# Optimization experiments

Measured on AMD Instinct MI355X. Metric: run time of the kernel, lower is better.

Reference implementation:

```python
import jax, jax.numpy as jnp
import numpy as np

N, E, F, H, C = 50000, 800000, 128, 256, 40
BN_EPS = 1e-5


def setup_inputs() -> dict:
    key = jax.random.key(0)
    ks = jax.random.split(key, 8)
    s = 0.05
    return {
        'x': jax.random.normal(ks[0], (N, F), jnp.float32),
        'edge_index': jax.random.randint(ks[1], (2, E), 0, N),
        'eps1': jnp.zeros((), jnp.float32),
        'W1': jax.random.normal(ks[2], (F, H), jnp.float32) * s,
        'b1': jnp.zeros((H,), jnp.float32),
        'g1': jnp.ones((H,), jnp.float32),
        'be1': jnp.zeros((H,), jnp.float32),
        'W2': jax.random.normal(ks[3], (H, H), jnp.float32) * s,
        'b2': jnp.zeros((H,), jnp.float32),
        'eps2': jnp.zeros((), jnp.float32),
        'W3': jax.random.normal(ks[4], (H, H), jnp.float32) * s,
        'b3': jnp.zeros((H,), jnp.float32),
        'g2': jnp.ones((H,), jnp.float32),
        'be2': jnp.zeros((H,), jnp.float32),
        'W4': jax.random.normal(ks[5], (H, H), jnp.float32) * s,
        'b4': jnp.zeros((H,), jnp.float32),
        'g3': jnp.ones((H,), jnp.float32),
        'be3': jnp.zeros((H,), jnp.float32),
        'Wf': jax.random.normal(ks[6], (H, C), jnp.float32) * s,
        'bf': jnp.zeros((C,), jnp.float32),
    }


def _bn(h, g, b):
    # BatchNorm1d forward with batch statistics (training-mode math, biased var)
    m = jnp.mean(h, axis=0)
    v = jnp.var(h, axis=0)
    return (h - m) * jax.lax.rsqrt(v + BN_EPS) * g + b


def _gin_conv(x, edge_index, eps, Wa, ba, g, be, Wb, bb):
    # GINConv: out = mlp((1+eps)*x + sum_{(src->dst)} x[src])
    src, dst = edge_index[0], edge_index[1]
    agg = jax.ops.segment_sum(x[src], dst, num_segments=x.shape[0])  # [N, d]
    h = (1.0 + eps) * x + agg
    h = jnp.maximum(_bn(h @ Wa + ba, g, be), 0.0)  # Linear-BN-ReLU
    return h @ Wb + bb                              # Linear


def reference(x, edge_index, eps1, W1, b1, g1, be1, W2, b2,
              eps2, W3, b3, g2, be2, W4, b4, g3, be3, Wf, bf):
    h = _gin_conv(x, edge_index, eps1, W1, b1, g1, be1, W2, b2)
    h = jnp.maximum(h, 0.0)  # F.relu (dropout p=0)
    h = _gin_conv(h, edge_index, eps2, W3, b3, g2, be2, W4, b4)
    h = jnp.maximum(_bn(h, g3, be3), 0.0)  # bn2 + relu
    return h @ Wf + bf  # fc -> [N, C]
```

## Files before the change

### kernel.cpp

```cpp
#include <hip/hip_runtime.h>
#include <hip/hip_bf16.h>


#define NN 50000
#define EE 800000
#define FDIM 128
#define HDIM 256
#define CDIM 40
#define BN_EPS 1e-5f
#define CSTRIDE 136

typedef unsigned short u16;
typedef unsigned int u32;
typedef __attribute__((ext_vector_type(8))) short short8;
typedef __attribute__((ext_vector_type(4))) float f32x4;

__device__ __forceinline__ float bflo(u32 u) { return __uint_as_float(u << 16); }
__device__ __forceinline__ float bfhi(u32 u) { return __uint_as_float(u & 0xFFFF0000u); }
__device__ __forceinline__ u16 f2bf(float f) {
  __hip_bfloat16 h = __float2bfloat16(f);
  return *(u16*)&h;
}
__device__ __forceinline__ u32 pack2(float a, float b) {
  return (u32)f2bf(a) | ((u32)f2bf(b) << 16);
}

__global__ void k_hist(const int* __restrict__ ei, int* __restrict__ deg) {
  int e = blockIdx.x * 256 + threadIdx.x;
  if (e < EE) atomicAdd(&deg[ei[EE + e]], 1);
}

__global__ void k_scan_blocks(const int* __restrict__ in, int* __restrict__ partial,
                              int* __restrict__ bsums, int n) {
  __shared__ int s[256];
  int i = blockIdx.x * 256 + threadIdx.x;
  s[threadIdx.x] = (i < n) ? in[i] : 0;
  __syncthreads();
  for (int d = 1; d < 256; d <<= 1) {
    int t = (threadIdx.x >= d) ? s[threadIdx.x - d] : 0;
    __syncthreads();
    s[threadIdx.x] += t;
    __syncthreads();
  }
  if (i < n) partial[i] = s[threadIdx.x];
  if (threadIdx.x == 255) bsums[blockIdx.x] = s[255];
}

__global__ void k_scan_sums(int* __restrict__ bs, int nb) {
  __shared__ int s[256];
  s[threadIdx.x] = (threadIdx.x < nb) ? bs[threadIdx.x] : 0;
  __syncthreads();
  for (int d = 1; d < 256; d <<= 1) {
    int t = (threadIdx.x >= d) ? s[threadIdx.x - d] : 0;
    __syncthreads();
    s[threadIdx.x] += t;
    __syncthreads();
  }
  int ex = (threadIdx.x == 0) ? 0 : s[threadIdx.x - 1];
  if (threadIdx.x < nb) bs[threadIdx.x] = ex;
}

__global__ void k_scan_add(const int* __restrict__ partial, const int* __restrict__ bs,
                           int* __restrict__ rowstart, int n) {
  int i = blockIdx.x * 256 + threadIdx.x;
  if (i < n) rowstart[i + 1] = partial[i] + bs[blockIdx.x];
  if (i == 0) rowstart[0] = 0;
}

__global__ void k_copy_i32(const int* __restrict__ a, int* __restrict__ b, int n) {
  int i = blockIdx.x * 256 + threadIdx.x;
  if (i < n) b[i] = a[i];
}

__global__ void k_scatter(const int* __restrict__ ei, int* __restrict__ cursor,
                          int* __restrict__ sorted_src) {
  int e = blockIdx.x * 256 + threadIdx.x;
  if (e < EE) {
    int dst = ei[EE + e];
    int p = atomicAdd(&cursor[dst], 1);
    sorted_src[p] = ei[e];
  }
}

__global__ void k_cvt_x(const float* __restrict__ x, u16* __restrict__ xb) {
  int i = blockIdx.x * 256 + threadIdx.x;
  size_t base = (size_t)i * 4;
  if (base < (size_t)NN * FDIM) {
    float4 v = *(const float4*)&x[base];
    u32 lo = pack2(v.x, v.y), hi = pack2(v.z, v.w);
    *(uint2*)&xb[base] = make_uint2(lo, hi);
  }
}

__global__ void k_cvt_wt(const float* __restrict__ W, u16* __restrict__ Wt, int K) {
  int i = blockIdx.x * 256 + threadIdx.x;
  int k = i >> 8, n = i & 255;
  if (k < K) Wt[(size_t)n * K + k] = f2bf(W[i]);
}

template <int FEAT>
__global__ __launch_bounds__(256)
void k_agg(const u16* __restrict__ x, const int* __restrict__ rowstart,
           const int* __restrict__ sorted_src, const float* __restrict__ epsp,
           u16* __restrict__ out) {
  int node = blockIdx.x * 4 + (threadIdx.x >> 6);
  if (node >= NN) return;
  int lane = threadIdx.x & 63;
  float e1 = 1.0f + epsp[0];
  int s = rowstart[node], t = rowstart[node + 1];
  if constexpr (FEAT == 128) {
    const u32* xp = (const u32*)x;
    u32 u = xp[(size_t)node * 64 + lane];
    float a0 = bflo(u) * e1, a1 = bfhi(u) * e1;
    int p = s;
    for (; p + 7 < t; p += 8) {
      u32 uu[8];
#pragma unroll
      for (int i = 0; i < 8; ++i) uu[i] = xp[(size_t)sorted_src[p + i] * 64 + lane];
#pragma unroll
      for (int i = 0; i < 8; ++i) { a0 += bflo(uu[i]); a1 += bfhi(uu[i]); }
    }
    for (; p + 1 < t; p += 2) {
      u32 u0 = xp[(size_t)sorted_src[p] * 64 + lane];
      u32 u1 = xp[(size_t)sorted_src[p + 1] * 64 + lane];
      a0 += bflo(u0) + bflo(u1);
      a1 += bfhi(u0) + bfhi(u1);
    }
    if (p < t) {
      u32 u0 = xp[(size_t)sorted_src[p] * 64 + lane];
      a0 += bflo(u0); a1 += bfhi(u0);
    }
    ((u32*)out)[(size_t)node * 64 + lane] = pack2(a0, a1);
  } else {
    const uint2* xp = (const uint2*)x;
    uint2 u = xp[(size_t)node * 64 + lane];
    float a0 = bflo(u.x) * e1, a1 = bfhi(u.x) * e1;
    float a2 = bflo(u.y) * e1, a3 = bfhi(u.y) * e1;
    int p = s;
    for (; p + 7 < t; p += 8) {
      uint2 uu[8];
#pragma unroll
      for (int i = 0; i < 8; ++i) uu[i] = xp[(size_t)sorted_src[p + i] * 64 + lane];
#pragma unroll
      for (int i = 0; i < 8; ++i) {
        a0 += bflo(uu[i].x); a1 += bfhi(uu[i].x);
        a2 += bflo(uu[i].y); a3 += bfhi(uu[i].y);
      }
    }
    for (; p + 1 < t; p += 2) {
      uint2 u0 = xp[(size_t)sorted_src[p] * 64 + lane];
      uint2 u1 = xp[(size_t)sorted_src[p + 1] * 64 + lane];
      a0 += bflo(u0.x) + bflo(u1.x);
      a1 += bfhi(u0.x) + bfhi(u1.x);
      a2 += bflo(u0.y) + bflo(u1.y);
      a3 += bfhi(u0.y) + bfhi(u1.y);
    }
    if (p < t) {
      uint2 u0 = xp[(size_t)sorted_src[p] * 64 + lane];
      a0 += bflo(u0.x); a1 += bfhi(u0.x);
      a2 += bflo(u0.y); a3 += bfhi(u0.y);
    }
    ((uint2*)out)[(size_t)node * 64 + lane] = make_uint2(pack2(a0, a1), pack2(a2, a3));
  }
}

template <int K, bool TRANSFORM, bool RELU_OUT, bool COLSUMS>
__global__ __launch_bounds__(256)
void k_gemm(const u16* __restrict__ A, const u16* __restrict__ Bt,
            const float* __restrict__ bias, const float* __restrict__ ta,
            const float* __restrict__ tc, u16* __restrict__ C,
            float* __restrict__ csum, float* __restrict__ csq) {
  constexpr int NCH = K / 8;
  constexpr int NKS = K / 32;
  constexpr int NTILE = (NN + 31) / 32;
  __shared__ u16 Bs[128 * K];
  __shared__ u16 Cs[32 * CSTRIDE];
  __shared__ float2 Tb[K];

  const int tid = threadIdx.x;
  const int lane = tid & 63;
  const int w = tid >> 6;
  const int wm = w >> 1, wn = w & 1;
  const int lr = lane & 15, lq = lane >> 4;
  const int half = blockIdx.x & 1;
  const u16* Bth = Bt + (size_t)half * 128 * K;

  for (int i = tid; i < 128 * NCH; i += 256) {
    int row = i / NCH, c = i % NCH;
    short8 v = *(const short8*)&Bth[(size_t)row * K + c * 8];
    ((short8*)Bs)[row * NCH + (c ^ (row & 7))] = v;
  }
  if constexpr (TRANSFORM) {
    for (int k = tid; k < K; k += 256) Tb[k] = make_float2(ta[k], tc[k]);
  }

  float bv[4];
#pragma unroll
  for (int ni = 0; ni < 4; ++ni) bv[ni] = bias[half * 128 + wn * 64 + ni * 16 + lr];
  float colS[4] = {}, colQ[4] = {};

  __syncthreads();

  short8 bufA[NKS], bufB[NKS];

  auto LOADA = [&](short8* dst, int rt) {
    int row = rt * 32 + wm * 16 + lr;
    int rowc = row < NN ? row : NN - 1;
    const u16* Ap = &A[(size_t)rowc * K];
#pragma unroll
    for (int ks = 0; ks < NKS; ++ks)
      dst[ks] = *(const short8*)&Ap[ks * 32 + lq * 8];
  };

  auto BODY = [&](short8* cur, short8* nxt, int rt) {
    if constexpr (TRANSFORM) {
#pragma unroll
      for (int ks = 0; ks < NKS; ++ks) {
        short8 v = cur[ks];
#pragma unroll
        for (int j = 0; j < 8; ++j) {
          float2 tb = Tb[ks * 32 + lq * 8 + j];
          float f = __uint_as_float(((u32)(u16)v[j]) << 16);
          v[j] = (short)f2bf(fmaxf(fmaf(f, tb.x, tb.y), 0.f));
        }
        cur[ks] = v;
      }
    }
    if (rt + 256 < NTILE) LOADA(nxt, rt + 256);

    f32x4 acc[4];
#pragma unroll
    for (int ni = 0; ni < 4; ++ni) acc[ni] = (f32x4){0.f, 0.f, 0.f, 0.f};
    __builtin_amdgcn_s_setprio(1);
#pragma unroll
    for (int ks = 0; ks < NKS; ++ks) {
#pragma unroll
      for (int ni = 0; ni < 4; ++ni) {
        int col = wn * 64 + ni * 16 + lr;
        int c = (ks * 4 + lq) ^ (col & 7);
        short8 bfr = ((const short8*)Bs)[col * NCH + c];
        acc[ni] = __builtin_amdgcn_mfma_f32_16x16x32_bf16(cur[ks], bfr, acc[ni], 0, 0, 0);
      }
    }
    __builtin_amdgcn_s_setprio(0);

#pragma unroll
    for (int ni = 0; ni < 4; ++ni) {
      int col = wn * 64 + ni * 16 + lr;
#pragma unroll
      for (int j = 0; j < 4; ++j) {
        int r = wm * 16 + lq * 4 + j;
        float v = acc[ni][j] + bv[ni];
        if constexpr (RELU_OUT) v = fmaxf(v, 0.f);
        if constexpr (COLSUMS) {
          if (rt * 32 + r < NN) { colS[ni] += v; colQ[ni] += v * v; }
        }
        Cs[r * CSTRIDE + col] = f2bf(v);
      }
    }
    __syncthreads();
    {
      int r = tid >> 3;
      int gr = rt * 32 + r;
      if (gr < NN) {
        const uint4* src = (const uint4*)&Cs[r * CSTRIDE + (tid & 7) * 16];
        uint4 v0 = src[0], v1 = src[1];
        uint4* dst = (uint4*)&C[(size_t)gr * HDIM + half * 128 + (tid & 7) * 16];
        dst[0] = v0; dst[1] = v1;
      }
    }
    __syncthreads();
  };

  LOADA(bufA, blockIdx.x >> 1);
  for (int rt = blockIdx.x >> 1; rt < NTILE; rt += 512) {
    BODY(bufA, bufB, rt);
    if (rt + 256 < NTILE) BODY(bufB, bufA, rt + 256);
  }

  if constexpr (COLSUMS) {
#pragma unroll
    for (int ni = 0; ni < 4; ++ni) {
      float s = colS[ni], q = colQ[ni];
      s += __shfl_xor(s, 16); s += __shfl_xor(s, 32);
      q += __shfl_xor(q, 16); q += __shfl_xor(q, 32);
      if (lq == 0) {
        int col = half * 128 + wn * 64 + ni * 16 + lr;
        atomicAdd(&csum[col], s);
        atomicAdd(&csq[col], q);
      }
    }
  }
}

__global__ void k_bn_fin(const float* __restrict__ sum, const float* __restrict__ sq,
                         const float* __restrict__ g, const float* __restrict__ be,
                         float* __restrict__ a, float* __restrict__ c) {
  int t = threadIdx.x;
  float m = sum[t] * (1.0f / NN);
  float var = sq[t] * (1.0f / NN) - m * m;
  float s = g[t] * rsqrtf(var + BN_EPS);
  a[t] = s;
  c[t] = be[t] - m * s;
}

__global__ __launch_bounds__(256)
void k_gemm_final(const u16* __restrict__ A, const float* __restrict__ B,
                  const float* __restrict__ bias, const float* __restrict__ ta,
                  const float* __restrict__ tc, float* __restrict__ C) {
  __shared__ float As[64][65];
  __shared__ float Bs[64][CDIM];
  int tid = threadIdx.x;
  int r = tid & 63, q = tid >> 6;
  int r0 = blockIdx.x * 64;
  float acc[10] = {};
  for (int k0 = 0; k0 < HDIM; k0 += 64) {
#pragma unroll
    for (int i = 0; i < 4; ++i) {
      int idx = tid + i * 256;
      int row = idx >> 4;
      int c4 = (idx & 15) * 4;
      int gr = r0 + row;
      float v0 = 0.f, v1 = 0.f, v2 = 0.f, v3 = 0.f;
      if (gr < NN) {
        uint2 u = *(const uint2*)&A[(size_t)gr * HDIM + k0 + c4];
        v0 = fmaxf(fmaf(bflo(u.x), ta[k0 + c4 + 0], tc[k0 + c4 + 0]), 0.f);
        v1 = fmaxf(fmaf(bfhi(u.x), ta[k0 + c4 + 1], tc[k0 + c4 + 1]), 0.f);
        v2 = fmaxf(fmaf(bflo(u.y), ta[k0 + c4 + 2], tc[k0 + c4 + 2]), 0.f);
        v3 = fmaxf(fmaf(bfhi(u.y), ta[k0 + c4 + 3], tc[k0 + c4 + 3]), 0.f);
      }
      As[c4 + 0][row] = v0;
      As[c4 + 1][row] = v1;
      As[c4 + 2][row] = v2;
      As[c4 + 3][row] = v3;
    }
#pragma unroll
    for (int i = 0; i < 10; ++i) {
      int idx = tid + i * 256;
      int row = idx / CDIM;
      int col = idx % CDIM;
      Bs[row][col] = B[(size_t)(k0 + row) * CDIM + col];
    }
    __syncthreads();
#pragma unroll
    for (int k = 0; k < 64; ++k) {
      float a = As[k][r];
#pragma unroll
      for (int j = 0; j < 10; ++j) acc[j] = fmaf(a, Bs[k][q * 10 + j], acc[j]);
    }
    __syncthreads();
  }
  int gr = r0 + r;
  if (gr < NN) {
#pragma unroll
    for (int j = 0; j < 10; ++j) C[(size_t)gr * CDIM + q * 10 + j] = acc[j] + bias[q * 10 + j];
  }
}

extern "C" void kernel_launch(void* const* d_in, const int* in_sizes, int n_in,
                              void* d_out, int out_size, void* d_ws, size_t ws_size,
                              hipStream_t stream) {
  const float* x   = (const float*)d_in[0];
  const int*   ei  = (const int*)d_in[1];
  const float* eps1= (const float*)d_in[2];
  const float* W1  = (const float*)d_in[3];
  const float* b1  = (const float*)d_in[4];
  const float* g1  = (const float*)d_in[5];
  const float* be1 = (const float*)d_in[6];
  const float* W2  = (const float*)d_in[7];
  const float* b2  = (const float*)d_in[8];
  const float* eps2= (const float*)d_in[9];
  const float* W3  = (const float*)d_in[10];
  const float* b3  = (const float*)d_in[11];
  const float* g2  = (const float*)d_in[12];
  const float* be2 = (const float*)d_in[13];
  const float* W4  = (const float*)d_in[14];
  const float* b4  = (const float*)d_in[15];
  const float* g3  = (const float*)d_in[16];
  const float* be3 = (const float*)d_in[17];
  const float* Wf  = (const float*)d_in[18];
  const float* bf  = (const float*)d_in[19];
  float* out = (float*)d_out;

  char* p = (char*)d_ws;
  auto alloc = [&](size_t bytes) -> char* {
    char* r = p;
    p += (bytes + 255) & ~(size_t)255;
    return r;
  };
  float* stats   = (float*)alloc(12 * 256 * sizeof(float));
  int* deg       = (int*)alloc(NN * sizeof(int));
  int* rowstart  = (int*)alloc((NN + 16) * sizeof(int));
  int* cursor    = (int*)alloc(NN * sizeof(int));
  int* sorted    = (int*)alloc(EE * sizeof(int));
  int* partial   = (int*)alloc(NN * sizeof(int));
  int* bsums     = (int*)alloc(1024 * sizeof(int));
  u16* W1t       = (u16*)alloc(256 * 128 * sizeof(u16));
  u16* W2t       = (u16*)alloc(256 * 256 * sizeof(u16));
  u16* W3t       = (u16*)alloc(256 * 256 * sizeof(u16));
  u16* W4t       = (u16*)alloc(256 * 256 * sizeof(u16));
  u16* xb        = (u16*)alloc((size_t)NN * 128 * sizeof(u16));
  u16* A1        = (u16*)alloc((size_t)NN * 128 * sizeof(u16));
  u16* z1        = (u16*)alloc((size_t)NN * 256 * sizeof(u16));
  u16* h1        = (u16*)alloc((size_t)NN * 256 * sizeof(u16));
  u16* A2        = (u16*)alloc((size_t)NN * 256 * sizeof(u16));
  (void)alloc(64 * 1024);
  u16* z2 = z1;
  u16* z3 = h1;

  hipMemsetAsync(deg, 0, NN * sizeof(int), stream);
  hipMemsetAsync(stats, 0, 12 * 256 * sizeof(float), stream);

  const int nbE = (EE + 255) / 256;
  const int nbN = (NN + 255) / 256;

  k_hist<<<nbE, 256, 0, stream>>>(ei, deg);
  k_scan_blocks<<<nbN, 256, 0, stream>>>(deg, partial, bsums, NN);
  k_scan_sums<<<1, 256, 0, stream>>>(bsums, nbN);
  k_scan_add<<<nbN, 256, 0, stream>>>(partial, bsums, rowstart, NN);
  k_copy_i32<<<nbN, 256, 0, stream>>>(rowstart, cursor, NN);
  k_scatter<<<nbE, 256, 0, stream>>>(ei, cursor, sorted);

  k_cvt_x<<<(NN * FDIM / 4 + 255) / 256, 256, 0, stream>>>(x, xb);
  k_cvt_wt<<<128, 256, 0, stream>>>(W1, W1t, 128);
  k_cvt_wt<<<256, 256, 0, stream>>>(W2, W2t, 256);
  k_cvt_wt<<<256, 256, 0, stream>>>(W3, W3t, 256);
  k_cvt_wt<<<256, 256, 0, stream>>>(W4, W4t, 256);

  k_agg<128><<<(NN + 3) / 4, 256, 0, stream>>>(xb, rowstart, sorted, eps1, A1);
  k_gemm<128, false, false, true><<<512, 256, 0, stream>>>(
      A1, W1t, b1, nullptr, nullptr, z1, stats + 0, stats + 256);
  k_bn_fin<<<1, 256, 0, stream>>>(stats + 0, stats + 256, g1, be1,
                                  stats + 2 * 256, stats + 3 * 256);
  k_gemm<256, true, true, false><<<512, 256, 0, stream>>>(
      z1, W2t, b2, stats + 2 * 256, stats + 3 * 256, h1, nullptr, nullptr);

  k_agg<256><<<(NN + 3) / 4, 256, 0, stream>>>(h1, rowstart, sorted, eps2, A2);
  k_gemm<256, false, false, true><<<512, 256, 0, stream>>>(
      A2, W3t, b3, nullptr, nullptr, z2, stats + 4 * 256, stats + 5 * 256);
  k_bn_fin<<<1, 256, 0, stream>>>(stats + 4 * 256, stats + 5 * 256, g2, be2,
                                  stats + 6 * 256, stats + 7 * 256);
  k_gemm<256, true, false, true><<<512, 256, 0, stream>>>(
      z2, W4t, b4, stats + 6 * 256, stats + 7 * 256, z3, stats + 8 * 256, stats + 9 * 256);
  k_bn_fin<<<1, 256, 0, stream>>>(stats + 8 * 256, stats + 9 * 256, g3, be3,
                                  stats + 10 * 256, stats + 11 * 256);

  k_gemm_final<<<(NN + 63) / 64, 256, 0, stream>>>(
      z3, Wf, bf, stats + 10 * 256, stats + 11 * 256, out);
}
```

Measured before the change: 391.4 us.

## Fuse neighbor aggregation into GEMM, fold BN finalize, use MFMA for final layer

The edge aggregation now runs inside a new 1024-thread GEMM kernel that gathers 32 rows into shared memory and multiplies them there, which removes the A1/A2 intermediate round trips through global memory. The BN finalize kernels are folded into the consuming GEMMs, the weight conversions are merged into a single launch, and the final fp32 FMA GEMM is replaced by a bf16 MFMA kernel using a padded transposed Wf. The cost is a 1024-thread block holding the full B matrix in LDS, which lowers occupancy and ties the gather latency to each tile's MFMA schedule. The final layer also gains an extra bf16 rounding.

Measured after the change: 378.3 us. 1.03x faster.

```diff
diff --git a/kernel.cpp b/kernel.cpp
--- a/kernel.cpp
+++ b/kernel.cpp
@@ -87,89 +87,234 @@
   size_t base = (size_t)i * 4;
   if (base < (size_t)NN * FDIM) {
     float4 v = *(const float4*)&x[base];
-    u32 lo = pack2(v.x, v.y), hi = pack2(v.z, v.w);
-    *(uint2*)&xb[base] = make_uint2(lo, hi);
-  }
-}
-
-__global__ void k_cvt_wt(const float* __restrict__ W, u16* __restrict__ Wt, int K) {
-  int i = blockIdx.x * 256 + threadIdx.x;
-  int k = i >> 8, n = i & 255;
-  if (k < K) Wt[(size_t)n * K + k] = f2bf(W[i]);
-}
-
-template <int FEAT>
-__global__ __launch_bounds__(256)
-void k_agg(const u16* __restrict__ x, const int* __restrict__ rowstart,
-           const int* __restrict__ sorted_src, const float* __restrict__ epsp,
-           u16* __restrict__ out) {
-  int node = blockIdx.x * 4 + (threadIdx.x >> 6);
-  if (node >= NN) return;
-  int lane = threadIdx.x & 63;
-  float e1 = 1.0f + epsp[0];
-  int s = rowstart[node], t = rowstart[node + 1];
-  if constexpr (FEAT == 128) {
-    const u32* xp = (const u32*)x;
-    u32 u = xp[(size_t)node * 64 + lane];
-    float a0 = bflo(u) * e1, a1 = bfhi(u) * e1;
-    int p = s;
-    for (; p + 7 < t; p += 8) {
-      u32 uu[8];
-#pragma unroll
-      for (int i = 0; i < 8; ++i) uu[i] = xp[(size_t)sorted_src[p + i] * 64 + lane];
-#pragma unroll
-      for (int i = 0; i < 8; ++i) { a0 += bflo(uu[i]); a1 += bfhi(uu[i]); }
-    }
-    for (; p + 1 < t; p += 2) {
-      u32 u0 = xp[(size_t)sorted_src[p] * 64 + lane];
-      u32 u1 = xp[(size_t)sorted_src[p + 1] * 64 + lane];
-      a0 += bflo(u0) + bflo(u1);
-      a1 += bfhi(u0) + bfhi(u1);
-    }
-    if (p < t) {
-      u32 u0 = xp[(size_t)sorted_src[p] * 64 + lane];
-      a0 += bflo(u0); a1 += bfhi(u0);
-    }
-    ((u32*)out)[(size_t)node * 64 + lane] = pack2(a0, a1);
+    *(uint2*)&xb[base] = make_uint2(pack2(v.x, v.y), pack2(v.z, v.w));
+  }
+}
+
+__global__ void k_cvt_w(const float* __restrict__ W1, const float* __restrict__ W2,
+                        const float* __restrict__ W3, const float* __restrict__ W4,
+                        const float* __restrict__ Wf,
+                        u16* __restrict__ W1t, u16* __restrict__ W2t,
+                        u16* __restrict__ W3t, u16* __restrict__ W4t,
+                        u16* __restrict__ Wft) {
+  int b = blockIdx.x, t = threadIdx.x;
+  if (b < 128) {
+    int i = b * 256 + t; int k = i >> 8, n = i & 255;
+    W1t[(size_t)n * 128 + k] = f2bf(W1[i]);
+  } else if (b < 384) {
+    int i = (b - 128) * 256 + t; int k = i >> 8, n = i & 255;
+    W2t[(size_t)n * 256 + k] = f2bf(W2[i]);
+  } else if (b < 640) {
+    int i = (b - 384) * 256 + t; int k = i >> 8, n = i & 255;
+    W3t[(size_t)n * 256 + k] = f2bf(W3[i]);
+  } else if (b < 896) {
+    int i = (b - 640) * 256 + t; int k = i >> 8, n = i & 255;
+    W4t[(size_t)n * 256 + k] = f2bf(W4[i]);
   } else {
-    const uint2* xp = (const uint2*)x;
-    uint2 u = xp[(size_t)node * 64 + lane];
-    float a0 = bflo(u.x) * e1, a1 = bfhi(u.x) * e1;
-    float a2 = bflo(u.y) * e1, a3 = bfhi(u.y) * e1;
-    int p = s;
-    for (; p + 7 < t; p += 8) {
-      uint2 uu[8];
-#pragma unroll
-      for (int i = 0; i < 8; ++i) uu[i] = xp[(size_t)sorted_src[p + i] * 64 + lane];
-#pragma unroll
-      for (int i = 0; i < 8; ++i) {
-        a0 += bflo(uu[i].x); a1 += bfhi(uu[i].x);
-        a2 += bflo(uu[i].y); a3 += bfhi(uu[i].y);
-      }
-    }
-    for (; p + 1 < t; p += 2) {
-      uint2 u0 = xp[(size_t)sorted_src[p] * 64 + lane];
-      uint2 u1 = xp[(size_t)sorted_src[p + 1] * 64 + lane];
-      a0 += bflo(u0.x) + bflo(u1.x);
-      a1 += bfhi(u0.x) + bfhi(u1.x);
-      a2 += bflo(u0.y) + bflo(u1.y);
-      a3 += bfhi(u0.y) + bfhi(u1.y);
-    }
-    if (p < t) {
-      uint2 u0 = xp[(size_t)sorted_src[p] * 64 + lane];
-      a0 += bflo(u0.x); a1 += bfhi(u0.x);
-      a2 += bflo(u0.y); a3 += bfhi(u0.y);
-    }
-    ((uint2*)out)[(size_t)node * 64 + lane] = make_uint2(pack2(a0, a1), pack2(a2, a3));
-  }
-}
-
-template <int K, bool TRANSFORM, bool RELU_OUT, bool COLSUMS>
+    int i = (b - 896) * 256 + t;
+    int c = i >> 8, k = i & 255;
+    Wft[(size_t)c * 256 + k] = (c < CDIM) ? f2bf(Wf[(size_t)k * CDIM + c]) : (u16)0;
+  }
+}
+
+template <int K>
+__global__ __launch_bounds__(1024)
+void k_fused(const u16* __restrict__ X, const int* __restrict__ rowstart,
+             const int* __restrict__ sorted_src, const float* __restrict__ epsp,
+             const u16* __restrict__ Bt, const float* __restrict__ bias,
+             u16* __restrict__ C, float* __restrict__ csum, float* __restrict__ csq) {
+  constexpr int NCH = K / 8;
+  constexpr bool DB = (K == 128);
+  constexpr int NTILE = (NN + 31) / 32;
+  __shared__ u16 Bs[256 * K];
+  __shared__ u16 As[DB ? 2 : 1][32 * K];
+  __shared__ u16 Cs[DB ? 32 * 272 : 8];
+
+  const int tid = threadIdx.x;
+  const int lane = tid & 63;
+  const int w = tid >> 6;
+  const int rg = w >> 3, cg = w & 7;
+  const int lr = lane & 15, lq = lane >> 4;
+
+  for (int i = tid; i < 256 * NCH; i += 1024) {
+    int row = i / NCH, c = i % NCH;
+    ((short8*)Bs)[row * NCH + (c ^ (row & 7))] = ((const short8*)Bt)[i];
+  }
+  const float e1 = 1.0f + epsp[0];
+  float bv[2];
+#pragma unroll
+  for (int ni = 0; ni < 2; ++ni) bv[ni] = bias[cg * 32 + ni * 16 + lr];
+  float colS[2] = {}, colQ[2] = {};
+
+  auto GATHER = [&](int grow, float* a) {
+    a[0] = a[1] = 0.f;
+    if constexpr (!DB) { a[2] = a[3] = 0.f; }
+    if (grow >= NN) return;
+    int s = rowstart[grow], t = rowstart[grow + 1];
+    if constexpr (!DB) {
+      const uint2* xp = (const uint2*)X;
+      uint2 u = xp[(size_t)grow * 64 + lane];
+      a[0] = bflo(u.x) * e1; a[1] = bfhi(u.x) * e1;
+      a[2] = bflo(u.y) * e1; a[3] = bfhi(u.y) * e1;
+      int p = s;
+      for (; p + 7 < t; p += 8) {
+        uint2 uu[8];
+#pragma unroll
+        for (int i = 0; i < 8; ++i) uu[i] = xp[(size_t)sorted_src[p + i] * 64 + lane];
+#pragma unroll
+        for (int i = 0; i < 8; ++i) {
+          a[0] += bflo(uu[i].x); a[1] += bfhi(uu[i].x);
+          a[2] += bflo(uu[i].y); a[3] += bfhi(uu[i].y);
+        }
+      }
+      for (; p < t; ++p) {
+        uint2 u0 = xp[(size_t)sorted_src[p] * 64 + lane];
+        a[0] += bflo(u0.x); a[1] += bfhi(u0.x);
+        a[2] += bflo(u0.y); a[3] += bfhi(u0.y);
+      }
+    } else {
+      const u32* xp = (const u32*)X;
+      u32 u = xp[(size_t)grow * 64 + lane];
+      a[0] = bflo(u) * e1; a[1] = bfhi(u) * e1;
+      int p = s;
+      for (; p + 7 < t; p += 8) {
+        u32 uu[8];
+#pragma unroll
+        for (int i = 0; i < 8; ++i) uu[i] = xp[(size_t)sorted_src[p + i] * 64 + lane];
+#pragma unroll
+        for (int i = 0; i < 8; ++i) { a[0] += bflo(uu[i]); a[1] += bfhi(uu[i]); }
+      }
+      for (; p < t; ++p) {
+        u32 u0 = xp[(size_t)sorted_src[p] * 64 + lane];
+        a[0] += bflo(u0); a[1] += bfhi(u0);
+      }
+    }
+  };
+
+  auto GWRITE = [&](u16* Abuf, int lw, const float* a) {
+    if constexpr (!DB) {
+      int idx = lw * 256 + (((lane >> 1) ^ (lw & 7)) << 3) + (lane & 1) * 4;
+      *(uint2*)&Abuf[idx] = make_uint2(pack2(a[0], a[1]), pack2(a[2], a[3]));
+    } else {
+      int idx = lw * 128 + (((lane >> 2) ^ (lw & 7)) << 3) + (lane & 3) * 2;
+      *(u32*)&Abuf[idx] = pack2(a[0], a[1]);
+    }
+  };
+
+  const int arow = rg * 16 + lr;
+  auto MFMA_TILE = [&](const u16* Abuf, f32x4* acc) {
+    acc[0] = (f32x4){0.f, 0.f, 0.f, 0.f};
+    acc[1] = (f32x4){0.f, 0.f, 0.f, 0.f};
+    __builtin_amdgcn_s_setprio(1);
+#pragma unroll
+    for (int ks = 0; ks < K / 32; ++ks) {
+      short8 af = *(const short8*)&Abuf[arow * K + (((ks * 4 + lq) ^ (arow & 7)) << 3)];
+#pragma unroll
+      for (int ni = 0; ni < 2; ++ni) {
+        int col = cg * 32 + ni * 16 + lr;
+        short8 bfr = ((const short8*)Bs)[col * NCH + ((ks * 4 + lq) ^ (col & 7))];
+        acc[ni] = __builtin_amdgcn_mfma_f32_16x16x32_bf16(af, bfr, acc[ni], 0, 0, 0);
+      }
+    }
+    __builtin_amdgcn_s_setprio(0);
+  };
+
+  const int rt0 = blockIdx.x;
+  float ga0[4], ga1[4];
+  GATHER(rt0 * 32 + w * 2 + 0, ga0);
+  GATHER(rt0 * 32 + w * 2 + 1, ga1);
+  GWRITE(As[0], w * 2 + 0, ga0);
+  GWRITE(As[0], w * 2 + 1, ga1);
+  __syncthreads();
+
+  int cur = 0;
+  for (int rt = rt0; rt < NTILE; rt += 256) {
+    f32x4 acc[2];
+    MFMA_TILE(As[cur], acc);
+    bool hn = (rt + 256) < NTILE;
+    if (hn) {
+      GATHER((rt + 256) * 32 + w * 2 + 0, ga0);
+      GATHER((rt + 256) * 32 + w * 2 + 1, ga1);
+    }
+    if constexpr (DB) {
+#pragma unroll
+      for (int ni = 0; ni < 2; ++ni) {
+        int col = cg * 32 + ni * 16 + lr;
+#pragma unroll
+        for (int j = 0; j < 4; ++j) {
+          int r = rg * 16 + lq * 4 + j;
+          float v = acc[ni][j] + bv[ni];
+          if (rt * 32 + r < NN) { colS[ni] += v; colQ[ni] += v * v; }
+          Cs[r * 272 + col] = f2bf(v);
+        }
+      }
+      if (hn) {
+        GWRITE(As[cur ^ 1], w * 2 + 0, ga0);
+        GWRITE(As[cur ^ 1], w * 2 + 1, ga1);
+      }
+      __syncthreads();
+      {
+        int r = tid >> 5, ch = tid & 31;
+        int gr = rt * 32 + r;
+        if (gr < NN) {
+          uint4 v = *(const uint4*)&Cs[r * 272 + ch * 8];
+          *(uint4*)&C[(size_t)gr * 256 + ch * 8] = v;
+        }
+      }
+      __syncthreads();
+      cur ^= 1;
+    } else {
+      __syncthreads();
+#pragma unroll
+      for (int ni = 0; ni < 2; ++ni) {
+        int col = cg * 32 + ni * 16 + lr;
+#pragma unroll
+        for (int j = 0; j < 4; ++j) {
+          int r = rg * 16 + lq * 4 + j;
+          float v = acc[ni][j] + bv[ni];
+          if (rt * 32 + r < NN) { colS[ni] += v; colQ[ni] += v * v; }
+          As[0][r * 256 + (((col >> 3) ^ (r & 7)) << 3) + (col & 7)] = f2bf(v);
+        }
+      }
+      __syncthreads();
+      {
+        int r = tid >> 5, ch = tid & 31;
+        int gr = rt * 32 + r;
+        if (gr < NN) {
+          uint4 v = *(const uint4*)&As[0][r * 256 + ((ch ^ (r & 7)) << 3)];
+          *(uint4*)&C[(size_t)gr * 256 + ch * 8] = v;
+        }
+      }
+      __syncthreads();
+      if (hn) {
+        GWRITE(As[0], w * 2 + 0, ga0);
+        GWRITE(As[0], w * 2 + 1, ga1);
+      }
+      __syncthreads();
+    }
+  }
+
+#pragma unroll
+  for (int ni = 0; ni < 2; ++ni) {
+    float s = colS[ni], q = colQ[ni];
+    s += __shfl_xor(s, 16); s += __shfl_xor(s, 32);
+    q += __shfl_xor(q, 16); q += __shfl_xor(q, 32);
+    if (lq == 0) {
+      int col = cg * 32 + ni * 16 + lr;
+      atomicAdd(&csum[col], s);
+      atomicAdd(&csq[col], q);
+    }
+  }
+}
+
+template <bool RELU_OUT, bool COLSUMS>
 __global__ __launch_bounds__(256)
 void k_gemm(const u16* __restrict__ A, const u16* __restrict__ Bt,
-            const float* __restrict__ bias, const float* __restrict__ ta,
-            const float* __restrict__ tc, u16* __restrict__ C,
-            float* __restrict__ csum, float* __restrict__ csq) {
+            const float* __restrict__ bias,
+            const float* __restrict__ icsum, const float* __restrict__ icsq,
+            const float* __restrict__ g, const float* __restrict__ be,
+            u16* __restrict__ C, float* __restrict__ ocsum, float* __restrict__ ocsq) {
+  constexpr int K = 256;
   constexpr int NCH = K / 8;
   constexpr int NKS = K / 32;
   constexpr int NTILE = (NN + 31) / 32;
@@ -190,8 +335,11 @@
     short8 v = *(const short8*)&Bth[(size_t)row * K + c * 8];
     ((short8*)Bs)[row * NCH + (c ^ (row & 7))] = v;
   }
-  if constexpr (TRANSFORM) {
-    for (int k = tid; k < K; k += 256) Tb[k] = make_float2(ta[k], tc[k]);
+  if (tid < 256) {
+    float m = icsum[tid] * (1.0f / NN);
+    float var = icsq[tid] * (1.0f / NN) - m * m;
+    float s = g[tid] * rsqrtf(var + BN_EPS);
+    Tb[tid] = make_float2(s, be[tid] - m * s);
   }
 
   float bv[4];
@@ -213,18 +361,16 @@
   };
 
   auto BODY = [&](short8* cur, short8* nxt, int rt) {
-    if constexpr (TRANSFORM) {
-#pragma unroll
-      for (int ks = 0; ks < NKS; ++ks) {
-        short8 v = cur[ks];
-#pragma unroll
-        for (int j = 0; j < 8; ++j) {
-          float2 tb = Tb[ks * 32 + lq * 8 + j];
-          float f = __uint_as_float(((u32)(u16)v[j]) << 16);
-          v[j] = (short)f2bf(fmaxf(fmaf(f, tb.x, tb.y), 0.f));
-        }
-        cur[ks] = v;
-      }
+#pragma unroll
+    for (int ks = 0; ks < NKS; ++ks) {
+      short8 v = cur[ks];
+#pragma unroll
+      for (int j = 0; j < 8; ++j) {
+        float2 tb = Tb[ks * 32 + lq * 8 + j];
+        float f = __uint_as_float(((u32)(u16)v[j]) << 16);
+        v[j] = (short)f2bf(fmaxf(fmaf(f, tb.x, tb.y), 0.f));
+      }
+      cur[ks] = v;
     }
     if (rt + 256 < NTILE) LOADA(nxt, rt + 256);
 
@@ -286,74 +432,78 @@
       q += __shfl_xor(q, 16); q += __shfl_xor(q, 32);
       if (lq == 0) {
         int col = half * 128 + wn * 64 + ni * 16 + lr;
-        atomicAdd(&csum[col], s);
-        atomicAdd(&csq[col], q);
-      }
-    }
-  }
-}
-
-__global__ void k_bn_fin(const float* __restrict__ sum, const float* __restrict__ sq,
-                         const float* __restrict__ g, const float* __restrict__ be,
-                         float* __restrict__ a, float* __restrict__ c) {
-  int t = threadIdx.x;
-  float m = sum[t] * (1.0f / NN);
-  float var = sq[t] * (1.0f / NN) - m * m;
-  float s = g[t] * rsqrtf(var + BN_EPS);
-  a[t] = s;
-  c[t] = be[t] - m * s;
+        atomicAdd(&ocsum[col], s);
+        atomicAdd(&ocsq[col], q);
+      }
+    }
+  }
 }
 
 __global__ __launch_bounds__(256)
-void k_gemm_final(const u16* __restrict__ A, const float* __restrict__ B,
-                  const float* __restrict__ bias, const float* __restrict__ ta,
-                  const float* __restrict__ tc, float* __restrict__ C) {
-  __shared__ float As[64][65];
-  __shared__ float Bs[64][CDIM];
-  int tid = threadIdx.x;
-  int r = tid & 63, q = tid >> 6;
-  int r0 = blockIdx.x * 64;
-  float acc[10] = {};
-  for (int k0 = 0; k0 < HDIM; k0 += 64) {
-#pragma unroll
-    for (int i = 0; i < 4; ++i) {
-      int idx = tid + i * 256;
-      int row = idx >> 4;
-      int c4 = (idx & 15) * 4;
-      int gr = r0 + row;
-      float v0 = 0.f, v1 = 0.f, v2 = 0.f, v3 = 0.f;
-      if (gr < NN) {
-        uint2 u = *(const uint2*)&A[(size_t)gr * HDIM + k0 + c4];
-        v0 = fmaxf(fmaf(bflo(u.x), ta[k0 + c4 + 0], tc[k0 + c4 + 0]), 0.f);
-        v1 = fmaxf(fmaf(bfhi(u.x), ta[k0 + c4 + 1], tc[k0 + c4 + 1]), 0.f);
-        v2 = fmaxf(fmaf(bflo(u.y), ta[k0 + c4 + 2], tc[k0 + c4 + 2]), 0.f);
-        v3 = fmaxf(fmaf(bfhi(u.y), ta[k0 + c4 + 3], tc[k0 + c4 + 3]), 0.f);
-      }
-      As[c4 + 0][row] = v0;
-      As[c4 + 1][row] = v1;
-      As[c4 + 2][row] = v2;
-      As[c4 + 3][row] = v3;
-    }
-#pragma unroll
-    for (int i = 0; i < 10; ++i) {
-      int idx = tid + i * 256;
-      int row = idx / CDIM;
-      int col = idx % CDIM;
-      Bs[row][col] = B[(size_t)(k0 + row) * CDIM + col];
-    }
-    __syncthreads();
-#pragma unroll
-    for (int k = 0; k < 64; ++k) {
-      float a = As[k][r];
-#pragma unroll
-      for (int j = 0; j < 10; ++j) acc[j] = fmaf(a, Bs[k][q * 10 + j], acc[j]);
-    }
-    __syncthreads();
-  }
-  int gr = r0 + r;
-  if (gr < NN) {
-#pragma unroll
-    for (int j = 0; j < 10; ++j) C[(size_t)gr * CDIM + q * 10 + j] = acc[j] + bias[q * 10 + j];
+void k_final(const u16* __restrict__ z3, const u16* __restrict__ Wft,
+             const float* __restrict__ bf,
+             const float* __restrict__ icsum, const float* __restrict__ icsq,
+             const float* __restrict__ g, const float* __restrict__ be,
+             float* __restrict__ out) {
+  __shared__ u16 Bs[48 * 256];
+  __shared__ float2 Tb[256];
+  const int tid = threadIdx.x;
+  const int lane = tid & 63;
+  const int w = tid >> 6;
+  const int lr = lane & 15, lq = lane >> 4;
+
+  for (int i = tid; i < 48 * 32; i += 256) {
+    int row = i >> 5, c = i & 31;
+    ((short8*)Bs)[row * 32 + (c ^ (row & 7))] = ((const short8*)Wft)[i];
+  }
+  if (tid < 256) {
+    float m = icsum[tid] * (1.0f / NN);
+    float var = icsq[tid] * (1.0f / NN) - m * m;
+    float s = g[tid] * rsqrtf(var + BN_EPS);
+    Tb[tid] = make_float2(s, be[tid] - m * s);
+  }
+  __syncthreads();
+
+  int row = blockIdx.x * 64 + w * 16 + lr;
+  int rowc = row < NN ? row : NN - 1;
+  const u16* Ap = &z3[(size_t)rowc * 256];
+  short8 a[8];
+#pragma unroll
+  for (int ks = 0; ks < 8; ++ks) {
+    short8 v = *(const short8*)&Ap[ks * 32 + lq * 8];
+#pragma unroll
+    for (int j = 0; j < 8; ++j) {
+      float2 tb = Tb[ks * 32 + lq * 8 + j];
+      float f = __uint_as_float(((u32)(u16)v[j]) << 16);
+      v[j] = (short)f2bf(fmaxf(fmaf(f, tb.x, tb.y), 0.f));
+    }
+    a[ks] = v;
+  }
+
+  f32x4 acc[3];
+#pragma unroll
+  for (int ni = 0; ni < 3; ++ni) acc[ni] = (f32x4){0.f, 0.f, 0.f, 0.f};
+#pragma unroll
+  for (int ks = 0; ks < 8; ++ks) {
+#pragma unroll
+    for (int ni = 0; ni < 3; ++ni) {
+      int col = ni * 16 + lr;
+      short8 bfr = ((const short8*)Bs)[col * 32 + ((ks * 4 + lq) ^ (col & 7))];
+      acc[ni] = __builtin_amdgcn_mfma_f32_16x16x32_bf16(a[ks], bfr, acc[ni], 0, 0, 0);
+    }
+  }
+
+#pragma unroll
+  for (int ni = 0; ni < 3; ++ni) {
+    int col = ni * 16 + lr;
+    if (col < CDIM) {
+      float bfv = bf[col];
+#pragma unroll
+      for (int j = 0; j < 4; ++j) {
+        int gr = blockIdx.x * 64 + w * 16 + lq * 4 + j;
+        if (gr < NN) out[(size_t)gr * CDIM + col] = acc[ni][j] + bfv;
+      }
+    }
   }
 }
 
@@ -388,7 +538,7 @@
     p += (bytes + 255) & ~(size_t)255;
     return r;
   };
-  float* stats   = (float*)alloc(12 * 256 * sizeof(float));
+  float* stats   = (float*)alloc(6 * 256 * sizeof(float));
   int* deg       = (int*)alloc(NN * sizeof(int));
   int* rowstart  = (int*)alloc((NN + 16) * sizeof(int));
   int* cursor    = (int*)alloc(NN * sizeof(int));
@@ -399,17 +549,20 @@
   u16* W2t       = (u16*)alloc(256 * 256 * sizeof(u16));
   u16* W3t       = (u16*)alloc(256 * 256 * sizeof(u16));
   u16* W4t       = (u16*)alloc(256 * 256 * sizeof(u16));
+  u16* Wft       = (u16*)alloc(48 * 256 * sizeof(u16));
   u16* xb        = (u16*)alloc((size_t)NN * 128 * sizeof(u16));
-  u16* A1        = (u16*)alloc((size_t)NN * 128 * sizeof(u16));
   u16* z1        = (u16*)alloc((size_t)NN * 256 * sizeof(u16));
   u16* h1        = (u16*)alloc((size_t)NN * 256 * sizeof(u16));
-  u16* A2        = (u16*)alloc((size_t)NN * 256 * sizeof(u16));
   (void)alloc(64 * 1024);
   u16* z2 = z1;
   u16* z3 = h1;
 
+  float* s1 = stats + 0,    *q1 = stats + 256;
+  float* s2 = stats + 512,  *q2 = stats + 768;
+  float* s3 = stats + 1024, *q3 = stats + 1280;
+
   hipMemsetAsync(deg, 0, NN * sizeof(int), stream);
-  hipMemsetAsync(stats, 0, 12 * 256 * sizeof(float), stream);
+  hipMemsetAsync(stats, 0, 6 * 256 * sizeof(float), stream);
 
   const int nbE = (EE + 255) / 256;
   const int nbN = (NN + 255) / 256;
@@ -422,29 +575,11 @@
   k_scatter<<<nbE, 256, 0, stream>>>(ei, cursor, sorted);
 
   k_cvt_x<<<(NN * FDIM / 4 + 255) / 256, 256, 0, stream>>>(x, xb);
-  k_cvt_wt<<<128, 256, 0, stream>>>(W1, W1t, 128);
-  k_cvt_wt<<<256, 256, 0, stream>>>(W2, W2t, 256);
-  k_cvt_wt<<<256, 256, 0, stream>>>(W3, W3t, 256);
-  k_cvt_wt<<<256, 256, 0, stream>>>(W4, W4t, 256);
-
-  k_agg<128><<<(NN + 3) / 4, 256, 0, stream>>>(xb, rowstart, sorted, eps1, A1);
-  k_gemm<128, false, false, true><<<512, 256, 0, stream>>>(
-      A1, W1t, b1, nullptr, nullptr, z1, stats + 0, stats + 256);
-  k_bn_fin<<<1, 256, 0, stream>>>(stats + 0, stats + 256, g1, be1,
-                                  stats + 2 * 256, stats + 3 * 256);
-  k_gemm<256, true, true, false><<<512, 256, 0, stream>>>(
-      z1, W2t, b2, stats + 2 * 256, stats + 3 * 256, h1, nullptr, nullptr);
-
-  k_agg<256><<<(NN + 3) / 4, 256, 0, stream>>>(h1, rowstart, sorted, eps2, A2);
-  k_gemm<256, false, false, true><<<512, 256, 0, stream>>>(
-      A2, W3t, b3, nullptr, nullptr, z2, stats + 4 * 256, stats + 5 * 256);
-  k_bn_fin<<<1, 256, 0, stream>>>(stats + 4 * 256, stats + 5 * 256, g2, be2,
-                                  stats + 6 * 256, stats + 7 * 256);
-  k_gemm<256, true, false, true><<<512, 256, 0, stream>>>(
-      z2, W4t, b4, stats + 6 * 256, stats + 7 * 256, z3, stats + 8 * 256, stats + 9 * 256);
-  k_bn_fin<<<1, 256, 0, stream>>>(stats + 8 * 256, stats + 9 * 256, g3, be3,
-                                  stats + 10 * 256, stats + 11 * 256);
-
-  k_gemm_final<<<(NN + 63) / 64, 256, 0, stream>>>(
-      z3, Wf, bf, stats + 10 * 256, stats + 11 * 256, out);
-}
+  k_cvt_w<<<944, 256, 0, stream>>>(W1, W2, W3, W4, Wf, W1t, W2t, W3t, W4t, Wft);
+
+  k_fused<128><<<256, 1024, 0, stream>>>(xb, rowstart, sorted, eps1, W1t, b1, z1, s1, q1);
+  k_gemm<true, false><<<512, 256, 0, stream>>>(z1, W2t, b2, s1, q1, g1, be1, h1, nullptr, nullptr);
+  k_fused<256><<<256, 1024, 0, stream>>>(h1, rowstart, sorted, eps2, W3t, b3, z2, s2, q2);
+  k_gemm<false, true><<<512, 256, 0, stream>>>(z2, W4t, b4, s2, q2, g2, be2, z3, s3, q3);
+  k_final<<<(NN + 63) / 64, 256, 0, stream>>>(z3, Wft, bf, s3, q3, g3, be3, out);
+}
```
